# Optimization experiments

Measured on AMD Instinct MI355X. Metric: run time of the kernel, lower is better.

The kernel has to match this reference:

```python
import jax, jax.numpy as jnp
import numpy as np
import math

N, T, D = 4, 2048, 1024

def setup_inputs() -> dict:
    key = jax.random.key(0)
    ks = jax.random.split(key, 14)
    s = 1.0 / math.sqrt(D)
    p = {
        'X':  jax.random.normal(ks[0], (N, T, D), jnp.float32),
        'Wq': jax.random.uniform(ks[1], (D, D), jnp.float32, -s, s),
        'bq': jax.random.uniform(ks[2], (D,), jnp.float32, -s, s),
        'Wk': jax.random.uniform(ks[3], (D, D), jnp.float32, -s, s),
        'bk': jax.random.uniform(ks[4], (D,), jnp.float32, -s, s),
        'Wv': jax.random.uniform(ks[5], (D, D), jnp.float32, -s, s),
        'bv': jax.random.uniform(ks[6], (D,), jnp.float32, -s, s),
        'W1': jax.random.uniform(ks[7], (D, D), jnp.float32, -s, s),
        'b1': jax.random.uniform(ks[8], (D,), jnp.float32, -s, s),
        'W2': jax.random.uniform(ks[9], (D, D), jnp.float32, -s, s),
        'b2': jax.random.uniform(ks[10], (D,), jnp.float32, -s, s),
        'W3': jax.random.uniform(ks[11], (D, D), jnp.float32, -s, s),
        'b3': jax.random.uniform(ks[12], (D,), jnp.float32, -s, s),
        'g1': jnp.ones((D,), jnp.float32),  'be1': jnp.zeros((D,), jnp.float32),
        'g2': jnp.ones((D,), jnp.float32),  'be2': jnp.zeros((D,), jnp.float32),
    }
    return p

def _layer_norm(x, g, b, eps=1e-5):
    mu = jnp.mean(x, axis=-1, keepdims=True)
    var = jnp.mean(jnp.square(x - mu), axis=-1, keepdims=True)
    return (x - mu) * jax.lax.rsqrt(var + eps) * g + b

def reference(X, Wq, bq, Wk, bk, Wv, bv, W1, b1, W2, b2, W3, b3, g1, be1, g2, be2):
    d = X.shape[-1]
    q = X @ Wq + bq                      # (N,T,Dq)
    k = X @ Wk + bk
    v = X @ Wv + bv
    scores = jnp.einsum('ntd,nsd->nts', q, k) / jnp.sqrt(jnp.asarray(d, X.dtype))
    attn = jax.nn.softmax(scores, axis=-1)   # full (N,T,T), as in source
    ctx = jnp.einsum('nts,nsd->ntd', attn, v)
    h = _layer_norm(ctx + X, g1, be1)
    m = jax.nn.relu(h @ W1 + b1)
    m = jax.nn.relu(m @ W2 + b2)
    m = m @ W3 + b3
    return _layer_norm(m + h, g2, be2)
```

## Files before the change

### kernel.cpp

```cpp
#include <hip/hip_runtime.h>
#include <hip/hip_bf16.h>


typedef __attribute__((ext_vector_type(8))) short short8;
typedef __attribute__((ext_vector_type(4))) short short4v;
typedef __attribute__((ext_vector_type(4))) float float4v;

#define DEVI static __device__ __forceinline__

DEVI float bf2f(short s) {
  union { unsigned u; float f; } c;
  c.u = ((unsigned)(unsigned short)s) << 16;
  return c.f;
}
DEVI short f2bf(float f) {
  union { __hip_bfloat16 h; short s; } c;
  c.h = __float2bfloat16(f);
  return c.s;
}
DEVI void gload_lds16(const void* g, void* l) {
  __builtin_amdgcn_global_load_lds(
      (const __attribute__((address_space(1))) void*)g,
      (__attribute__((address_space(3))) void*)l, 16, 0, 0);
}

#define MFMA16 __builtin_amdgcn_mfma_f32_16x16x32_bf16
#define CFENCE asm volatile("" ::: "memory")
#define SCHEDB __builtin_amdgcn_sched_barrier(0)

template <int NFB>
__global__ __launch_bounds__(512, 4) void gemmT(
    const short* __restrict__ A, const short* __restrict__ B,
    const float* __restrict__ bias, float alpha, void* __restrict__ Cout,
    int K, int lda, int ldb, int ldc,
    long sA, long sB, long sC, int flags)
{
  constexpr int BUFB = 16384 + NFB * 2048;
  __shared__ __attribute__((aligned(16))) char lds[3 * BUFB];

  const int tid  = threadIdx.x;
  const int lane = tid & 63;
  const int wid  = tid >> 6;
  const int wm = wid >> 1, wn = wid & 1;
  const int lr = lane & 15;
  const int kq = lane >> 4;

  const long m0 = (long)blockIdx.x * 256;
  const long n0 = (long)blockIdx.y * (NFB * 32);
  const short* Ab = A + (long)blockIdx.z * sA;
  const short* Bb = B + (long)blockIdx.z * sB;

  const int sc8 = (((tid & 3) ^ ((tid >> 3) & 3)) << 3);
  const short* pA0 = Ab + (m0 + (tid >> 2)) * (long)lda + sc8;
  const short* pA1 = Ab + (m0 + 128 + (tid >> 2)) * (long)lda + sc8;
  const short* pB  = Bb + (n0 + (tid >> 2)) * (long)ldb + sc8;

  char* ldsB = lds;
  const int dst0 = tid * 16;
  const bool bldr = tid < NFB * 128;

  auto stage = [&](int bs, int kt) {
    const long ko = (long)kt * 32;
    gload_lds16(pA0 + ko, ldsB + bs + dst0);
    gload_lds16(pA1 + ko, ldsB + bs + 8192 + dst0);
    if (bldr) gload_lds16(pB + ko, ldsB + bs + 16384 + dst0);
  };

  const int swz = ((kq ^ ((lr >> 1) & 3)) << 4);
  const int baseA = (wm * 64 + lr) * 64 + swz;
  const int baseB = 16384 + (wn * (NFB * 16) + lr) * 64 + swz;

  float4v acc[4][NFB];
#pragma unroll
  for (int m = 0; m < 4; ++m)
#pragma unroll
    for (int n = 0; n < NFB; ++n)
#pragma unroll
      for (int i = 0; i < 4; ++i) acc[m][n][i] = 0.f;

  const int NT = K >> 5;

  stage(0, 0);
  stage(BUFB, 1);
  if (wid < 2 * NFB) { asm volatile("s_waitcnt vmcnt(3)" ::: "memory"); }
  else               { asm volatile("s_waitcnt vmcnt(2)" ::: "memory"); }
  __builtin_amdgcn_s_barrier();
  CFENCE;

  int bsR = 0;
  int bsS = 2 * BUFB;

  for (int t = 0; t < NT; ++t) {
    if (t + 2 < NT) stage(bsS, t + 2);

    const char* rA = ldsB + (bsR + baseA);
    const char* rB = ldsB + (bsR + baseB);
    short8 a0 = *(const short8*)(rA);
    short8 a1 = *(const short8*)(rA + 1024);
    short8 a2 = *(const short8*)(rA + 2048);
    short8 a3 = *(const short8*)(rA + 3072);
    short8 bf[NFB];
#pragma unroll
    for (int n = 0; n < NFB; ++n) bf[n] = *(const short8*)(rB + n * 1024);

    asm volatile("s_waitcnt lgkmcnt(0)" ::: "memory");
    SCHEDB;
    __builtin_amdgcn_s_setprio(1);
#pragma unroll
    for (int n = 0; n < NFB; ++n) {
      acc[0][n] = MFMA16(a0, bf[n], acc[0][n], 0, 0, 0);
      acc[1][n] = MFMA16(a1, bf[n], acc[1][n], 0, 0, 0);
      acc[2][n] = MFMA16(a2, bf[n], acc[2][n], 0, 0, 0);
      acc[3][n] = MFMA16(a3, bf[n], acc[3][n], 0, 0, 0);
    }
    __builtin_amdgcn_s_setprio(0);

    if (t + 2 < NT) {
      if (wid < 2 * NFB) { asm volatile("s_waitcnt vmcnt(3)" ::: "memory"); }
      else               { asm volatile("s_waitcnt vmcnt(2)" ::: "memory"); }
    } else {
      asm volatile("s_waitcnt vmcnt(0)" ::: "memory");
    }
    __builtin_amdgcn_s_barrier();
    CFENCE;

    bsR = (bsR == 2 * BUFB) ? 0 : bsR + BUFB;
    bsS = (bsS == 2 * BUFB) ? 0 : bsS + BUFB;
  }

  const int dob = flags & 1, dor = flags & 2, f32o = flags & 4;
  float* Cf = (float*)Cout + (long)blockIdx.z * sC;
  short* Cb = (short*)Cout + (long)blockIdx.z * sC;
  const long r0 = m0 + wm * 64 + kq * 4;
  const long c0 = n0 + wn * (NFB * 16) + lr;
#pragma unroll
  for (int m = 0; m < 4; ++m)
#pragma unroll
    for (int n = 0; n < NFB; ++n) {
      const long c = c0 + n * 16;
      float bv = dob ? bias[c] : 0.f;
#pragma unroll
      for (int i = 0; i < 4; ++i) {
        const long r = r0 + m * 16 + i;
        float v = acc[m][n][i] * alpha + bv;
        if (dor) v = fmaxf(v, 0.f);
        if (f32o) Cf[r * ldc + c] = v;
        else      Cb[r * ldc + c] = f2bf(v);
      }
    }
}


__global__ __launch_bounds__(256) void cast_x_k(const float* __restrict__ X,
                                                short* __restrict__ Xb) {
  int i = blockIdx.x * 256 + threadIdx.x;
  float4v v = ((const float4v*)X)[i];
  short4v o;
#pragma unroll
  for (int j = 0; j < 4; ++j) o[j] = f2bf(v[j]);
  ((short4v*)Xb)[i] = o;
}

__global__ __launch_bounds__(256) void wcast_k(
    const float* __restrict__ Wq, const float* __restrict__ Wk,
    const float* __restrict__ Wv, const float* __restrict__ W1,
    const float* __restrict__ W2, const float* __restrict__ W3,
    const float* __restrict__ bq, const float* __restrict__ bk,
    const float* __restrict__ bv,
    short* __restrict__ Wqkvt, short* __restrict__ W1t,
    short* __restrict__ W2t, short* __restrict__ W3t,
    float* __restrict__ bqkv) {
  const int z = blockIdx.z;
  if (z == 6) {
    if (blockIdx.y != 0 || blockIdx.x >= 12) return;
    int i = blockIdx.x * 256 + threadIdx.x;
    bqkv[i] = i < 1024 ? bq[i] : (i < 2048 ? bk[i - 1024] : bv[i - 2048]);
    return;
  }
  const float* W = z == 0 ? Wq : z == 1 ? Wk : z == 2 ? Wv : z == 3 ? W1 : z == 4 ? W2 : W3;
  short* Wt = z == 0 ? Wqkvt : z == 1 ? Wqkvt + 1048576 : z == 2 ? Wqkvt + 2097152
            : z == 3 ? W1t : z == 4 ? W2t : W3t;
  __shared__ float tile[32][33];
  int tx = threadIdx.x & 31, ty = threadIdx.x >> 5;
  int c0 = blockIdx.x * 32, r0 = blockIdx.y * 32;
#pragma unroll
  for (int r = ty; r < 32; r += 8)
    tile[r][tx] = W[(long)(r0 + r) * 1024 + c0 + tx];
  __syncthreads();
#pragma unroll
  for (int r = ty; r < 32; r += 8)
    Wt[(long)(c0 + r) * 1024 + r0 + tx] = f2bf(tile[tx][r]);
}

__global__ __launch_bounds__(256) void tv_k(const short* __restrict__ qkv,
                                            short* __restrict__ vT) {
  __shared__ short tile[32][33];
  int b = blockIdx.z;
  int tx = threadIdx.x & 31, ty = threadIdx.x >> 5;
  int d0 = blockIdx.x * 32, t0 = blockIdx.y * 32;
#pragma unroll
  for (int r = ty; r < 32; r += 8)
    tile[r][tx] = qkv[((long)(b * 2048 + t0 + r)) * 3072 + 2048 + d0 + tx];
  __syncthreads();
#pragma unroll
  for (int r = ty; r < 32; r += 8)
    vT[(long)b * 2097152 + (long)(d0 + r) * 2048 + t0 + tx] = tile[tx][r];
}

__global__ __launch_bounds__(256) void softmax_k(short* __restrict__ s) {
  __shared__ float red[8];
  long r = blockIdx.x;
  short* p = s + r * 2048;
  int tid = threadIdx.x;
  short8 raw = *(short8*)&p[tid * 8];
  float v[8];
  float mx = -1e30f;
#pragma unroll
  for (int j = 0; j < 8; ++j) { v[j] = bf2f(raw[j]); mx = fmaxf(mx, v[j]); }
#pragma unroll
  for (int o = 32; o; o >>= 1) mx = fmaxf(mx, __shfl_xor(mx, o));
  if ((tid & 63) == 0) red[tid >> 6] = mx;
  __syncthreads();
  mx = fmaxf(fmaxf(red[0], red[1]), fmaxf(red[2], red[3]));
  float sum = 0.f;
#pragma unroll
  for (int j = 0; j < 8; ++j) { v[j] = __expf(v[j] - mx); sum += v[j]; }
#pragma unroll
  for (int o = 32; o; o >>= 1) sum += __shfl_xor(sum, o);
  if ((tid & 63) == 0) red[4 + (tid >> 6)] = sum;
  __syncthreads();
  float inv = 1.f / (red[4] + red[5] + red[6] + red[7]);
  short8 o8;
#pragma unroll
  for (int j = 0; j < 8; ++j) o8[j] = f2bf(v[j] * inv);
  *(short8*)&p[tid * 8] = o8;
}

__global__ __launch_bounds__(256) void addln_k(const float* __restrict__ a,
                                               const float* __restrict__ b,
                                               const float* __restrict__ g,
                                               const float* __restrict__ be,
                                               float* __restrict__ outf,
                                               short* __restrict__ outb) {
  __shared__ float red[8];
  long r = blockIdx.x;
  int tid = threadIdx.x;
  float4v va = ((const float4v*)(a + r * 1024))[tid];
  float4v vb = ((const float4v*)(b + r * 1024))[tid];
  float x[4]; float s = 0.f;
#pragma unroll
  for (int j = 0; j < 4; ++j) { x[j] = va[j] + vb[j]; s += x[j]; }
#pragma unroll
  for (int o = 32; o; o >>= 1) s += __shfl_xor(s, o);
  if ((tid & 63) == 0) red[tid >> 6] = s;
  __syncthreads();
  float mu = (red[0] + red[1] + red[2] + red[3]) * (1.f / 1024.f);
  float ss = 0.f;
#pragma unroll
  for (int j = 0; j < 4; ++j) { float d = x[j] - mu; ss += d * d; }
#pragma unroll
  for (int o = 32; o; o >>= 1) ss += __shfl_xor(ss, o);
  if ((tid & 63) == 0) red[4 + (tid >> 6)] = ss;
  __syncthreads();
  float var = (red[4] + red[5] + red[6] + red[7]) * (1.f / 1024.f);
  float rstd = rsqrtf(var + 1e-5f);
  float4v vg = ((const float4v*)g)[tid];
  float4v vbe = ((const float4v*)be)[tid];
  float4v y;
#pragma unroll
  for (int j = 0; j < 4; ++j) y[j] = (x[j] - mu) * rstd * vg[j] + vbe[j];
  ((float4v*)(outf + r * 1024))[tid] = y;
  if (outb) {
    short4v ob;
#pragma unroll
    for (int j = 0; j < 4; ++j) ob[j] = f2bf(y[j]);
    ((short4v*)(outb + r * 1024))[tid] = ob;
  }
}


extern "C" void kernel_launch(void* const* d_in, const int* in_sizes, int n_in,
                              void* d_out, int out_size, void* d_ws, size_t ws_size,
                              hipStream_t stream) {
  const float* X  = (const float*)d_in[0];
  const float* Wq = (const float*)d_in[1];
  const float* bq = (const float*)d_in[2];
  const float* Wk = (const float*)d_in[3];
  const float* bk = (const float*)d_in[4];
  const float* Wv = (const float*)d_in[5];
  const float* bv = (const float*)d_in[6];
  const float* W1 = (const float*)d_in[7];
  const float* b1 = (const float*)d_in[8];
  const float* W2 = (const float*)d_in[9];
  const float* b2 = (const float*)d_in[10];
  const float* W3 = (const float*)d_in[11];
  const float* b3 = (const float*)d_in[12];
  const float* g1  = (const float*)d_in[13];
  const float* be1 = (const float*)d_in[14];
  const float* g2  = (const float*)d_in[15];
  const float* be2 = (const float*)d_in[16];

  char* ws = (char*)d_ws;
  short* Xb     = (short*)(ws + 0);
  short* Wqkvt  = (short*)(ws + 16777216);
  short* W1t    = (short*)(ws + 23068672);
  short* W2t    = (short*)(ws + 25165824);
  short* W3t    = (short*)(ws + 27262976);
  float* bqkv   = (float*)(ws + 29360128);
  short* qkv    = (short*)(ws + 29372416);
  short* vT     = (short*)(ws + 79704064);
  short* scores = (short*)(ws + 96481280);
  float* ctx    = (float*)(ws + 29372416);
  float* h      = (float*)(ws + 96481280);
  short* hb     = (short*)(ws + 0);
  short* m1     = (short*)(ws + 29372416);
  short* m2     = (short*)(ws + 46149632);
  float* m3     = (float*)(ws + 62926848);
  float* out    = (float*)d_out;

  cast_x_k<<<8192, 256, 0, stream>>>(X, Xb);
  wcast_k<<<dim3(32, 32, 7), 256, 0, stream>>>(Wq, Wk, Wv, W1, W2, W3,
                                               bq, bk, bv,
                                               Wqkvt, W1t, W2t, W3t, bqkv);

  gemmT<3><<<dim3(32, 32, 1), 512, 0, stream>>>(
      Xb, Wqkvt, bqkv, 1.0f, qkv, 1024, 1024, 1024, 3072, 0, 0, 0, 1);

  tv_k<<<dim3(32, 64, 4), 256, 0, stream>>>(qkv, vT);

  gemmT<4><<<dim3(8, 16, 4), 512, 0, stream>>>(
      qkv, qkv + 1024, nullptr, 0.03125f, scores, 1024, 3072, 3072, 2048,
      (long)2048 * 3072, (long)2048 * 3072, (long)2048 * 2048, 0);

  softmax_k<<<8192, 256, 0, stream>>>(scores);

  gemmT<2><<<dim3(8, 16, 4), 512, 0, stream>>>(
      scores, vT, nullptr, 1.0f, ctx, 2048, 2048, 2048, 1024,
      (long)2048 * 2048, (long)1024 * 2048, (long)2048 * 1024, 4);

  addln_k<<<8192, 256, 0, stream>>>(ctx, X, g1, be1, h, hb);

  gemmT<2><<<dim3(32, 16, 1), 512, 0, stream>>>(
      hb, W1t, b1, 1.0f, m1, 1024, 1024, 1024, 1024, 0, 0, 0, 3);
  gemmT<2><<<dim3(32, 16, 1), 512, 0, stream>>>(
      m1, W2t, b2, 1.0f, m2, 1024, 1024, 1024, 1024, 0, 0, 0, 3);
  gemmT<2><<<dim3(32, 16, 1), 512, 0, stream>>>(
      m2, W3t, b3, 1.0f, m3, 1024, 1024, 1024, 1024, 0, 0, 0, 5);

  addln_k<<<8192, 256, 0, stream>>>(m3, h, g2, be2, out, nullptr);
}
```

Baseline: 327.6 us.

## Replace 8-wave GEMM with 4-wave 256x128 tile kernel for all matmuls

Replaces the templated 512-thread GEMM, with N-tile 64–128, by a single 256-thread kernel that computes a fixed 256x128 output tile. Each wave now owns a 128x64 sub-tile with 8x4 MFMA accumulators. This is meant to give more operand reuse per LDS read and fewer blocks per GEMM. In exchange it uses more registers per thread, allows only 2 blocks per CU, and fills the grid less on the smaller GEMMs (e.g. 32x8 blocks for the MLP layers).

```diff
diff --git a/kernel.cpp b/kernel.cpp
--- a/kernel.cpp
+++ b/kernel.cpp
@@ -28,14 +28,13 @@
 #define CFENCE asm volatile("" ::: "memory")
 #define SCHEDB __builtin_amdgcn_sched_barrier(0)
 
-template <int NFB>
-__global__ __launch_bounds__(512, 4) void gemmT(
+__global__ __launch_bounds__(256, 2) void gemmW(
     const short* __restrict__ A, const short* __restrict__ B,
     const float* __restrict__ bias, float alpha, void* __restrict__ Cout,
     int K, int lda, int ldb, int ldc,
     long sA, long sB, long sC, int flags)
 {
-  constexpr int BUFB = 16384 + NFB * 2048;
+  constexpr int BUFB = 24576;
   __shared__ __attribute__((aligned(16))) char lds[3 * BUFB];
 
   const int tid  = threadIdx.x;
@@ -46,35 +45,41 @@
   const int kq = lane >> 4;
 
   const long m0 = (long)blockIdx.x * 256;
-  const long n0 = (long)blockIdx.y * (NFB * 32);
+  const long n0 = (long)blockIdx.y * 128;
   const short* Ab = A + (long)blockIdx.z * sA;
   const short* Bb = B + (long)blockIdx.z * sB;
 
   const int sc8 = (((tid & 3) ^ ((tid >> 3) & 3)) << 3);
-  const short* pA0 = Ab + (m0 + (tid >> 2)) * (long)lda + sc8;
-  const short* pA1 = Ab + (m0 + 128 + (tid >> 2)) * (long)lda + sc8;
-  const short* pB  = Bb + (n0 + (tid >> 2)) * (long)ldb + sc8;
+  const int srow = tid >> 2;
+  const short* pA0 = Ab + (m0 + srow) * (long)lda + sc8;
+  const short* pA1 = Ab + (m0 + 64 + srow) * (long)lda + sc8;
+  const short* pA2 = Ab + (m0 + 128 + srow) * (long)lda + sc8;
+  const short* pA3 = Ab + (m0 + 192 + srow) * (long)lda + sc8;
+  const short* pB0 = Bb + (n0 + srow) * (long)ldb + sc8;
+  const short* pB1 = Bb + (n0 + 64 + srow) * (long)ldb + sc8;
 
   char* ldsB = lds;
   const int dst0 = tid * 16;
-  const bool bldr = tid < NFB * 128;
 
   auto stage = [&](int bs, int kt) {
     const long ko = (long)kt * 32;
     gload_lds16(pA0 + ko, ldsB + bs + dst0);
-    gload_lds16(pA1 + ko, ldsB + bs + 8192 + dst0);
-    if (bldr) gload_lds16(pB + ko, ldsB + bs + 16384 + dst0);
+    gload_lds16(pA1 + ko, ldsB + bs + 4096 + dst0);
+    gload_lds16(pA2 + ko, ldsB + bs + 8192 + dst0);
+    gload_lds16(pA3 + ko, ldsB + bs + 12288 + dst0);
+    gload_lds16(pB0 + ko, ldsB + bs + 16384 + dst0);
+    gload_lds16(pB1 + ko, ldsB + bs + 20480 + dst0);
   };
 
   const int swz = ((kq ^ ((lr >> 1) & 3)) << 4);
-  const int baseA = (wm * 64 + lr) * 64 + swz;
-  const int baseB = 16384 + (wn * (NFB * 16) + lr) * 64 + swz;
-
-  float4v acc[4][NFB];
-#pragma unroll
-  for (int m = 0; m < 4; ++m)
-#pragma unroll
-    for (int n = 0; n < NFB; ++n)
+  const int baseA = (wm * 128 + lr) * 64 + swz;
+  const int baseB = 16384 + (wn * 64 + lr) * 64 + swz;
+
+  float4v acc[8][4];
+#pragma unroll
+  for (int m = 0; m < 8; ++m)
+#pragma unroll
+    for (int n = 0; n < 4; ++n)
 #pragma unroll
       for (int i = 0; i < 4; ++i) acc[m][n][i] = 0.f;
 
@@ -82,8 +87,7 @@
 
   stage(0, 0);
   stage(BUFB, 1);
-  if (wid < 2 * NFB) { asm volatile("s_waitcnt vmcnt(3)" ::: "memory"); }
-  else               { asm volatile("s_waitcnt vmcnt(2)" ::: "memory"); }
+  asm volatile("s_waitcnt vmcnt(6)" ::: "memory");
   __builtin_amdgcn_s_barrier();
   CFENCE;
 
@@ -95,32 +99,24 @@
 
     const char* rA = ldsB + (bsR + baseA);
     const char* rB = ldsB + (bsR + baseB);
-    short8 a0 = *(const short8*)(rA);
-    short8 a1 = *(const short8*)(rA + 1024);
-    short8 a2 = *(const short8*)(rA + 2048);
-    short8 a3 = *(const short8*)(rA + 3072);
-    short8 bf[NFB];
-#pragma unroll
-    for (int n = 0; n < NFB; ++n) bf[n] = *(const short8*)(rB + n * 1024);
+    short8 af[8], bf[4];
+#pragma unroll
+    for (int m = 0; m < 8; ++m) af[m] = *(const short8*)(rA + m * 1024);
+#pragma unroll
+    for (int n = 0; n < 4; ++n) bf[n] = *(const short8*)(rB + n * 1024);
 
     asm volatile("s_waitcnt lgkmcnt(0)" ::: "memory");
     SCHEDB;
     __builtin_amdgcn_s_setprio(1);
 #pragma unroll
-    for (int n = 0; n < NFB; ++n) {
-      acc[0][n] = MFMA16(a0, bf[n], acc[0][n], 0, 0, 0);
-      acc[1][n] = MFMA16(a1, bf[n], acc[1][n], 0, 0, 0);
-      acc[2][n] = MFMA16(a2, bf[n], acc[2][n], 0, 0, 0);
-      acc[3][n] = MFMA16(a3, bf[n], acc[3][n], 0, 0, 0);
-    }
+    for (int m = 0; m < 8; ++m)
+#pragma unroll
+      for (int n = 0; n < 4; ++n)
+        acc[m][n] = MFMA16(af[m], bf[n], acc[m][n], 0, 0, 0);
     __builtin_amdgcn_s_setprio(0);
 
-    if (t + 2 < NT) {
-      if (wid < 2 * NFB) { asm volatile("s_waitcnt vmcnt(3)" ::: "memory"); }
-      else               { asm volatile("s_waitcnt vmcnt(2)" ::: "memory"); }
-    } else {
-      asm volatile("s_waitcnt vmcnt(0)" ::: "memory");
-    }
+    if (t + 2 < NT) { asm volatile("s_waitcnt vmcnt(6)" ::: "memory"); }
+    else            { asm volatile("s_waitcnt vmcnt(0)" ::: "memory"); }
     __builtin_amdgcn_s_barrier();
     CFENCE;
 
@@ -131,12 +127,12 @@
   const int dob = flags & 1, dor = flags & 2, f32o = flags & 4;
   float* Cf = (float*)Cout + (long)blockIdx.z * sC;
   short* Cb = (short*)Cout + (long)blockIdx.z * sC;
-  const long r0 = m0 + wm * 64 + kq * 4;
-  const long c0 = n0 + wn * (NFB * 16) + lr;
-#pragma unroll
-  for (int m = 0; m < 4; ++m)
-#pragma unroll
-    for (int n = 0; n < NFB; ++n) {
+  const long r0 = m0 + wm * 128 + kq * 4;
+  const long c0 = n0 + wn * 64 + lr;
+#pragma unroll
+  for (int m = 0; m < 8; ++m)
+#pragma unroll
+    for (int n = 0; n < 4; ++n) {
       const long c = c0 + n * 16;
       float bv = dob ? bias[c] : 0.f;
 #pragma unroll
@@ -323,28 +319,28 @@
                                                bq, bk, bv,
                                                Wqkvt, W1t, W2t, W3t, bqkv);
 
-  gemmT<3><<<dim3(32, 32, 1), 512, 0, stream>>>(
+  gemmW<<<dim3(32, 24, 1), 256, 0, stream>>>(
       Xb, Wqkvt, bqkv, 1.0f, qkv, 1024, 1024, 1024, 3072, 0, 0, 0, 1);
 
   tv_k<<<dim3(32, 64, 4), 256, 0, stream>>>(qkv, vT);
 
-  gemmT<4><<<dim3(8, 16, 4), 512, 0, stream>>>(
+  gemmW<<<dim3(8, 16, 4), 256, 0, stream>>>(
       qkv, qkv + 1024, nullptr, 0.03125f, scores, 1024, 3072, 3072, 2048,
       (long)2048 * 3072, (long)2048 * 3072, (long)2048 * 2048, 0);
 
   softmax_k<<<8192, 256, 0, stream>>>(scores);
 
-  gemmT<2><<<dim3(8, 16, 4), 512, 0, stream>>>(
+  gemmW<<<dim3(8, 8, 4), 256, 0, stream>>>(
       scores, vT, nullptr, 1.0f, ctx, 2048, 2048, 2048, 1024,
       (long)2048 * 2048, (long)1024 * 2048, (long)2048 * 1024, 4);
 
   addln_k<<<8192, 256, 0, stream>>>(ctx, X, g1, be1, h, hb);
 
-  gemmT<2><<<dim3(32, 16, 1), 512, 0, stream>>>(
+  gemmW<<<dim3(32, 8, 1), 256, 0, stream>>>(
       hb, W1t, b1, 1.0f, m1, 1024, 1024, 1024, 1024, 0, 0, 0, 3);
-  gemmT<2><<<dim3(32, 16, 1), 512, 0, stream>>>(
+  gemmW<<<dim3(32, 8, 1), 256, 0, stream>>>(
       m1, W2t, b2, 1.0f, m2, 1024, 1024, 1024, 1024, 0, 0, 0, 3);
-  gemmT<2><<<dim3(32, 16, 1), 512, 0, stream>>>(
+  gemmW<<<dim3(32, 8, 1), 256, 0, stream>>>(
       m2, W3t, b3, 1.0f, m3, 1024, 1024, 1024, 1024, 0, 0, 0, 5);
 
   addln_k<<<8192, 256, 0, stream>>>(m3, h, g2, be2, out, nullptr);
```

Result: slower. 344.2 us (+5.1%).
